# Kernel tuning notes

Measured on AMD Instinct MI355X. Metric: run time of the kernel, lower is better.

## Reference

```python
import jax, jax.numpy as jnp
import numpy as np

NUM_LATENTS = 1
NUM_EMBEDDINGS = 2048
EMBEDDING_DIM = 64
DECAY = 0.99
EPS = 1e-5


def setup_inputs() -> dict:
    key = jax.random.key(0)
    k1, k2 = jax.random.split(key)
    x = jax.random.normal(k1, (65536, NUM_LATENTS * EMBEDDING_DIM), dtype=jnp.float32)
    embedding = jax.random.normal(k2, (NUM_LATENTS, NUM_EMBEDDINGS, EMBEDDING_DIM), dtype=jnp.float32)
    cluster_size = jnp.ones((NUM_LATENTS, NUM_EMBEDDINGS), dtype=jnp.float32)
    return {"input": x, "embedding": embedding, "cluster_size": cluster_size}


def reference(input, embedding, cluster_size):
    L, K, D = embedding.shape
    flat = input.reshape(-1, L, D)  # (N, L, D)
    # Squared euclidean distances (N, L, K), expanded form of (x - e)^2 sum over D
    x_sq = jnp.sum(flat * flat, axis=-1, keepdims=True)           # (N, L, 1)
    e_sq = jnp.sum(embedding * embedding, axis=-1)[None]          # (1, L, K)
    cross = jnp.einsum('nld,lkd->nlk', flat, embedding)           # (N, L, K)
    distances = x_sq - 2.0 * cross + e_sq
    encoding_indices = jnp.argmin(distances, axis=-1)             # (N, L)
    # decode: gather codebook vectors
    quantized = embedding[jnp.arange(L)[None, :], encoding_indices]  # (N, L, D)
    encodings = jax.nn.one_hot(encoding_indices, K, dtype=input.dtype)  # (N, L, K)
    # --- EMA update (training branch, non-simple, laplace smoothing) ---
    onehot_sum = jnp.sum(encodings, axis=0)                       # (L, K)
    dw = jnp.einsum('nlk,nld->lkd', encodings, flat)              # (L, K, D)
    new_cluster_size = DECAY * cluster_size + (1.0 - DECAY) * onehot_sum
    n = jnp.sum(new_cluster_size, axis=-1, keepdims=True)
    cs = (new_cluster_size + EPS) / (n + K * EPS) * n
    new_embedding = DECAY * embedding + (1.0 - DECAY) * (dw / cs[..., None])
    # --- losses / outputs ---
    q = quantized.reshape(input.shape)
    commitment_loss = jnp.mean((q - input) ** 2)
    quantized_st = input + jax.lax.stop_gradient(q - input)
    avg_probs = jnp.mean(encodings, axis=0)                       # (L, K)
    perplexity = jnp.exp(-jnp.sum(avg_probs * jnp.log(avg_probs + 1e-10) / L))
    return (quantized_st, encodings, commitment_loss, perplexity, new_embedding, new_cluster_size)
```

## Files before the change

kernel.cpp:

```cpp
#include <hip/hip_runtime.h>
#include <math.h>

#define NROWS 65536
#define KEMB  2048
#define DIM   64
#define DECAYF 0.99f
#define OMDF   0.01f
#define EPSF   1e-5f

#define WS_DW    0
#define WS_CNT   131072
#define WS_LOSS  133120
#define WS_ESQ   133632
#define WS_IDX   137728
#define WS_SORT  203264
#define WS_START 268800
#define WS_CUR   270852

#define OUT_Q    0
#define OUT_ENC  4194304
#define OUT_LOSS 138412032
#define OUT_PERP 138412033
#define OUT_NE   138412034
#define OUT_NCS  138543106

typedef float f32x4 __attribute__((ext_vector_type(4)));

__global__ __launch_bounds__(256) void k0_prep(const float* __restrict__ E,
                                               float* __restrict__ ws) {
    int g = blockIdx.x * 256 + threadIdx.x;
    if (g == 0) ws[WS_LOSS] = 0.f;
    ((float4*)(ws + WS_DW))[g] = make_float4(0.f, 0.f, 0.f, 0.f);
    if (g < KEMB) {
        ((unsigned int*)ws)[WS_CNT + g] = 0u;
        const float4* e4 = (const float4*)(E + (size_t)g * DIM);
        float s0 = 0.f, s1 = 0.f, s2 = 0.f, s3 = 0.f;
#pragma unroll
        for (int j = 0; j < 16; j++) {
            float4 v = e4[j];
            s0 = fmaf(v.x, v.x, s0); s1 = fmaf(v.y, v.y, s1);
            s2 = fmaf(v.z, v.z, s2); s3 = fmaf(v.w, v.w, s3);
        }
        ws[WS_ESQ + g] = (s0 + s1) + (s2 + s3);
    }
}

__global__ __launch_bounds__(256, 3) void k1_main(const float* __restrict__ x,
                                                  const float* __restrict__ E,
                                                  float* __restrict__ ws,
                                                  float* __restrict__ out) {
    __shared__ float sxT[64 * 128];
    __shared__ float seT[16 * 256];
    __shared__ float sxq[256];

    const int t = threadIdx.x;
    const int b = blockIdx.x;
    const int tx = t & 15;
    const int ty = t >> 4;

    {
        const int rl = t & 127;
        const int dhi2 = t >> 7;
        const float4* x4 = (const float4*)x;
        float s0 = 0.f, s1 = 0.f, s2 = 0.f, s3 = 0.f;
#pragma unroll
        for (int i = 0; i < 8; i++) {
            int dc = dhi2 + 2 * i;
            float4 v = x4[((size_t)b * 128 + rl) * 16 + dc];
            sxT[(4 * dc + 0) * 128 + rl] = v.x;
            sxT[(4 * dc + 1) * 128 + rl] = v.y;
            sxT[(4 * dc + 2) * 128 + rl] = v.z;
            sxT[(4 * dc + 3) * 128 + rl] = v.w;
            s0 = fmaf(v.x, v.x, s0); s1 = fmaf(v.y, v.y, s1);
            s2 = fmaf(v.z, v.z, s2); s3 = fmaf(v.w, v.w, s3);
        }
        sxq[dhi2 * 128 + rl] = (s0 + s1) + (s2 + s3);
    }

    const int sbase = (((t >> 2) & 3) << 6) + ((t >> 4) << 2) + (t & 3);
    const float4* e4 = (const float4*)E;

    float4 pv[4];
#pragma unroll
    for (int j = 0; j < 4; j++)
        pv[j] = e4[(size_t)t * 16 + j];

    __syncthreads();

    float xsq[8];
#pragma unroll
    for (int rr = 0; rr < 8; rr++)
        xsq[rr] = sxq[ty * 8 + rr] + sxq[128 + ty * 8 + rr];

    float best[8];
    int bidx[8];
#pragma unroll
    for (int rr = 0; rr < 8; rr++) { best[rr] = 3.4e38f; bidx[rr] = 0; }

    f32x4* __restrict__ encz = (f32x4*)(out + OUT_ENC);

    for (int pass = 0; pass < 8; pass++) {
        float acc[8][16];
#pragma unroll
        for (int rr = 0; rr < 8; rr++)
#pragma unroll
            for (int m = 0; m < 16; m++) acc[rr][m] = 0.f;

        for (int q = 0; q < 4; q++) {
            if (pass + q) __syncthreads();
#pragma unroll
            for (int j = 0; j < 4; j++) {
                seT[(4 * j + 0) * 256 + sbase] = pv[j].x;
                seT[(4 * j + 1) * 256 + sbase] = pv[j].y;
                seT[(4 * j + 2) * 256 + sbase] = pv[j].z;
                seT[(4 * j + 3) * 256 + sbase] = pv[j].w;
            }
            __syncthreads();

            {
                int h = pass * 4 + q + 1;
                if (h < 32) {
#pragma unroll
                    for (int j = 0; j < 4; j++)
                        pv[j] = e4[((size_t)((h >> 2) * 256 + t)) * 16 + (h & 3) * 4 + j];
                }
            }

            {
                f32x4 z = (f32x4)(0.f);
#pragma unroll
                for (int j = 0; j < 8; j++)
                    __builtin_nontemporal_store(z,
                        encz + (size_t)b * 65536 + pass * 8192 + (q * 8 + j) * 256 + t);
            }

            const float* xbase = sxT + q * 16 * 128 + ty * 8;
            for (int dd = 0; dd < 16; dd++) {
                const float* sb = seT + dd * 256;
                f32x4 a0 = *(const f32x4*)(xbase + dd * 128);
                f32x4 a1 = *(const f32x4*)(xbase + dd * 128 + 4);
                f32x4 b0 = *(const f32x4*)(sb + tx * 4);
                f32x4 b1 = *(const f32x4*)(sb + 64 + tx * 4);
                f32x4 b2 = *(const f32x4*)(sb + 128 + tx * 4);
                f32x4 b3 = *(const f32x4*)(sb + 192 + tx * 4);
#pragma unroll
                for (int rr = 0; rr < 4; rr++) {
#pragma unroll
                    for (int cc = 0; cc < 4; cc++) {
                        acc[rr][cc]          = fmaf(a0[rr], b0[cc], acc[rr][cc]);
                        acc[rr][4 + cc]      = fmaf(a0[rr], b1[cc], acc[rr][4 + cc]);
                        acc[rr][8 + cc]      = fmaf(a0[rr], b2[cc], acc[rr][8 + cc]);
                        acc[rr][12 + cc]     = fmaf(a0[rr], b3[cc], acc[rr][12 + cc]);
                        acc[4 + rr][cc]      = fmaf(a1[rr], b0[cc], acc[4 + rr][cc]);
                        acc[4 + rr][4 + cc]  = fmaf(a1[rr], b1[cc], acc[4 + rr][4 + cc]);
                        acc[4 + rr][8 + cc]  = fmaf(a1[rr], b2[cc], acc[4 + rr][8 + cc]);
                        acc[4 + rr][12 + cc] = fmaf(a1[rr], b3[cc], acc[4 + rr][12 + cc]);
                    }
                }
            }
        }

        const float4* esq4 = (const float4*)(ws + WS_ESQ + pass * 256 + tx * 16);
        float4 eqv0 = esq4[0], eqv1 = esq4[1], eqv2 = esq4[2], eqv3 = esq4[3];
        float eq[16] = {eqv0.x, eqv0.y, eqv0.z, eqv0.w, eqv1.x, eqv1.y, eqv1.z, eqv1.w,
                        eqv2.x, eqv2.y, eqv2.z, eqv2.w, eqv3.x, eqv3.y, eqv3.z, eqv3.w};
        const int kb = pass * 256 + tx * 16;
#pragma unroll
        for (int rr = 0; rr < 8; rr++)
#pragma unroll
            for (int m = 0; m < 16; m++) {
                float dist = fmaf(-2.f, acc[rr][m], xsq[rr]) + eq[m];
                if (dist < best[rr]) { best[rr] = dist; bidx[rr] = kb + m; }
            }
    }

    int* sIdx = (int*)sxq;
#pragma unroll
    for (int rr = 0; rr < 8; rr++) {
        float bd = best[rr]; int bi = bidx[rr];
#pragma unroll
        for (int m = 1; m < 16; m <<= 1) {
            float od = __shfl_xor(bd, m, 64);
            int   oi = __shfl_xor(bi, m, 64);
            if (od < bd || (od == bd && oi < bi)) { bd = od; bi = oi; }
        }
        if (tx == 0) sIdx[ty * 8 + rr] = bi;
    }
    __syncthreads();

    if (t < 128) {
        const int row = b * 128 + t;
        const int bi = sIdx[t];
        ((int*)ws)[WS_IDX + row] = bi;
        atomicAdd(((unsigned int*)ws) + WS_CNT + bi, 1u);
        out[OUT_ENC + (size_t)row * KEMB + bi] = 1.0f;
        const float4* ebb = (const float4*)(E + (size_t)bi * DIM);
        const float4* xr4 = (const float4*)(x + (size_t)row * DIM);
        float4* qo = (float4*)(out + OUT_Q + (size_t)row * DIM);
        float l0 = 0.f, l1 = 0.f, l2 = 0.f, l3 = 0.f;
#pragma unroll
        for (int j = 0; j < 16; j++) {
            float4 ev = ebb[j];
            float4 xv = xr4[j];
            qo[j] = ev;
            float d0 = ev.x - xv.x, d1 = ev.y - xv.y;
            float d2 = ev.z - xv.z, d3 = ev.w - xv.w;
            l0 = fmaf(d0, d0, l0); l1 = fmaf(d1, d1, l1);
            l2 = fmaf(d2, d2, l2); l3 = fmaf(d3, d3, l3);
        }
        float lsum = (l0 + l1) + (l2 + l3);
#pragma unroll
        for (int o = 32; o; o >>= 1) lsum += __shfl_down(lsum, o, 64);
        if ((t & 63) == 0) unsafeAtomicAdd(ws + WS_LOSS, lsum);
    }
}

__global__ __launch_bounds__(256) void k2scan(float* __restrict__ ws) {
    __shared__ unsigned int sscan[256];
    const int t = threadIdx.x;
    const unsigned int* cnt = ((const unsigned int*)ws) + WS_CNT;
    unsigned int c[8];
    unsigned int tot = 0;
#pragma unroll
    for (int j = 0; j < 8; j++) { c[j] = cnt[t * 8 + j]; tot += c[j]; }
    sscan[t] = tot;
    __syncthreads();
    for (int off = 1; off < 256; off <<= 1) {
        unsigned int v = (t >= off) ? sscan[t - off] : 0u;
        __syncthreads();
        sscan[t] += v;
        __syncthreads();
    }
    unsigned int run = sscan[t] - tot;
    unsigned int* starts = ((unsigned int*)ws) + WS_START;
    unsigned int* cur = ((unsigned int*)ws) + WS_CUR;
#pragma unroll
    for (int j = 0; j < 8; j++) {
        starts[t * 8 + j] = run;
        cur[t * 8 + j] = run;
        run += c[j];
    }
    if (t == 255) starts[KEMB] = run;
}

__global__ __launch_bounds__(256) void k2c_scatter(const int* __restrict__ idxp,
                                                   float* __restrict__ ws) {
    const int g = blockIdx.x * 256 + threadIdx.x;
    const int code = idxp[g];
    unsigned int p = atomicAdd(((unsigned int*)ws) + WS_CUR + code, 1u);
    ((int*)ws)[WS_SORT + p] = g;
}

__global__ __launch_bounds__(256) void k2d_dw(const float* __restrict__ x,
                                              const int* __restrict__ idxp,
                                              float* __restrict__ ws) {
    const int t = threadIdx.x;
    const int lane = t & 63;
    const int w = blockIdx.x * 4 + (t >> 6);
    const int base = w * 32;
    const int* sorted = ((const int*)ws) + WS_SORT;

    int rid = (lane < 32) ? sorted[base + lane] : 0;
    int code_l = (lane < 32) ? idxp[rid] : 0;

    float acc = 0.f;
    int cur = __shfl(code_l, 0, 64);
#pragma unroll 8
    for (int i = 0; i < 32; i++) {
        int row = __shfl(rid, i, 64);
        int code = __shfl(code_l, i, 64);
        if (code != cur) {
            unsafeAtomicAdd(ws + WS_DW + (size_t)cur * DIM + lane, acc);
            acc = 0.f;
            cur = code;
        }
        acc += x[(size_t)row * DIM + lane];
    }
    unsafeAtomicAdd(ws + WS_DW + (size_t)cur * DIM + lane, acc);
}

__global__ __launch_bounds__(256) void k3_se(const float* __restrict__ cs_in,
                                             const float* __restrict__ E,
                                             const float* __restrict__ ws,
                                             float* __restrict__ out) {
    __shared__ float sred[8];
    __shared__ float sscale[16];
    __shared__ float s_n;
    const int t = threadIdx.x;
    const int b = blockIdx.x;
    const unsigned int* cnt = ((const unsigned int*)ws) + WS_CNT;

    float ln = 0.f, lent = 0.f;
#pragma unroll
    for (int j = 0; j < 8; j++) {
        int k = t * 8 + j;
        float c = (float)cnt[k];
        float ncs = DECAYF * cs_in[k] + OMDF * c;
        ln += ncs;
        float p = c * (1.0f / 65536.0f);
        lent = fmaf(p, logf(p + 1e-10f), lent);
    }
#pragma unroll
    for (int o = 32; o; o >>= 1) {
        ln += __shfl_down(ln, o, 64);
        lent += __shfl_down(lent, o, 64);
    }
    if ((t & 63) == 0) { sred[t >> 6] = ln; sred[4 + (t >> 6)] = lent; }
    __syncthreads();
    if (t == 0) {
        float n = (sred[0] + sred[1]) + (sred[2] + sred[3]);
        float ent = (sred[4] + sred[5]) + (sred[6] + sred[7]);
        s_n = n;
        if (b == 0) {
            out[OUT_LOSS] = ws[WS_LOSS] * (1.0f / 4194304.0f);
            out[OUT_PERP] = expf(-ent);
        }
    }
    __syncthreads();
    const float n = s_n;

    if (t < 16) {
        int k = b * 16 + t;
        float c = (float)cnt[k];
        float ncs = DECAYF * cs_in[k] + OMDF * c;
        out[OUT_NCS + k] = ncs;
        float cs = (ncs + EPSF) / (n + (float)KEMB * EPSF) * n;
        sscale[t] = OMDF / cs;
    }
    __syncthreads();

    const int k16 = t >> 4;
    const int d = (t & 15) * 4;
    const int k = b * 16 + k16;
    const float sc = sscale[k16];
    float4 e = ((const float4*)E)[k * 16 + (t & 15)];
    float4 dv = ((const float4*)(ws + WS_DW))[k * 16 + (t & 15)];
    float2 r0, r1;
    r0.x = fmaf(dv.x, sc, DECAYF * e.x);
    r0.y = fmaf(dv.y, sc, DECAYF * e.y);
    r1.x = fmaf(dv.z, sc, DECAYF * e.z);
    r1.y = fmaf(dv.w, sc, DECAYF * e.w);
    float2* o2 = (float2*)(out + OUT_NE);
    o2[(k * 64 + d) / 2 + 0] = r0;
    o2[(k * 64 + d) / 2 + 1] = r1;
}

extern "C" void kernel_launch(void* const* d_in, const int* in_sizes, int n_in,
                              void* d_out, int out_size, void* d_ws, size_t ws_size,
                              hipStream_t stream) {
    const float* x = (const float*)d_in[0];
    const float* E = (const float*)d_in[1];
    const float* cs = (const float*)d_in[2];
    float* out = (float*)d_out;
    float* ws = (float*)d_ws;
    const int* idxp = ((const int*)ws) + WS_IDX;

    hipLaunchKernelGGL(k0_prep, dim3(128), dim3(256), 0, stream, E, ws);
    hipLaunchKernelGGL(k1_main, dim3(512), dim3(256), 0, stream, x, E, ws, out);
    hipLaunchKernelGGL(k2scan, dim3(1), dim3(256), 0, stream, ws);
    hipLaunchKernelGGL(k2c_scatter, dim3(256), dim3(256), 0, stream, idxp, ws);
    hipLaunchKernelGGL(k2d_dw, dim3(512), dim3(256), 0, stream, x, idxp, ws);
    hipLaunchKernelGGL(k3_se, dim3(128), dim3(256), 0, stream, cs, E, ws, out);
}
```

Measured before the change: 340.3 us.

## Split codebook search across two blocks per row tile and merge in new kernel

The main distance kernel now launches twice as many blocks, and each block searches half of the codebook for its 128 rows. Each half writes its local best distance and index to scratch space (reusing the sort workspace and the new-embedding output region). A new finalize kernel picks the better half, then does the count atomics, one-hot write, quantized output and loss. The shared-memory codebook tile is also padded to 288 floats per row to reduce bank conflicts. This trades extra x loads, an extra launch and an extra scratch round-trip for more parallelism across the GPU's CUs.

New measurement: 355.1 us. +4.3%, slower.

```diff
diff --git a/kernel.cpp b/kernel.cpp
--- a/kernel.cpp
+++ b/kernel.cpp
@@ -50,11 +50,12 @@
                                                   float* __restrict__ ws,
                                                   float* __restrict__ out) {
     __shared__ float sxT[64 * 128];
-    __shared__ float seT[16 * 256];
+    __shared__ float seT[16 * 288];
     __shared__ float sxq[256];
 
     const int t = threadIdx.x;
-    const int b = blockIdx.x;
+    const int rb = blockIdx.x >> 1;
+    const int cb = blockIdx.x & 1;
     const int tx = t & 15;
     const int ty = t >> 4;
 
@@ -66,7 +67,7 @@
 #pragma unroll
         for (int i = 0; i < 8; i++) {
             int dc = dhi2 + 2 * i;
-            float4 v = x4[((size_t)b * 128 + rl) * 16 + dc];
+            float4 v = x4[((size_t)rb * 128 + rl) * 16 + dc];
             sxT[(4 * dc + 0) * 128 + rl] = v.x;
             sxT[(4 * dc + 1) * 128 + rl] = v.y;
             sxT[(4 * dc + 2) * 128 + rl] = v.z;
@@ -77,13 +78,13 @@
         sxq[dhi2 * 128 + rl] = (s0 + s1) + (s2 + s3);
     }
 
-    const int sbase = (((t >> 2) & 3) << 6) + ((t >> 4) << 2) + (t & 3);
+    const int sbase = ((t >> 2) & 3) * 72 + ((t >> 4) << 2) + (t & 3);
     const float4* e4 = (const float4*)E;
 
     float4 pv[4];
 #pragma unroll
     for (int j = 0; j < 4; j++)
-        pv[j] = e4[(size_t)t * 16 + j];
+        pv[j] = e4[(size_t)(cb * 1024 + t) * 16 + j];
 
     __syncthreads();
 
@@ -99,7 +100,7 @@
 
     f32x4* __restrict__ encz = (f32x4*)(out + OUT_ENC);
 
-    for (int pass = 0; pass < 8; pass++) {
+    for (int pass = 0; pass < 4; pass++) {
         float acc[8][16];
 #pragma unroll
         for (int rr = 0; rr < 8; rr++)
@@ -107,22 +108,23 @@
             for (int m = 0; m < 16; m++) acc[rr][m] = 0.f;
 
         for (int q = 0; q < 4; q++) {
-            if (pass + q) __syncthreads();
+            const int st = pass * 4 + q;
+            if (st) __syncthreads();
 #pragma unroll
             for (int j = 0; j < 4; j++) {
-                seT[(4 * j + 0) * 256 + sbase] = pv[j].x;
-                seT[(4 * j + 1) * 256 + sbase] = pv[j].y;
-                seT[(4 * j + 2) * 256 + sbase] = pv[j].z;
-                seT[(4 * j + 3) * 256 + sbase] = pv[j].w;
+                seT[(4 * j + 0) * 288 + sbase] = pv[j].x;
+                seT[(4 * j + 1) * 288 + sbase] = pv[j].y;
+                seT[(4 * j + 2) * 288 + sbase] = pv[j].z;
+                seT[(4 * j + 3) * 288 + sbase] = pv[j].w;
             }
             __syncthreads();
 
             {
-                int h = pass * 4 + q + 1;
-                if (h < 32) {
+                int h = st + 1;
+                if (h < 16) {
 #pragma unroll
                     for (int j = 0; j < 4; j++)
-                        pv[j] = e4[((size_t)((h >> 2) * 256 + t)) * 16 + (h & 3) * 4 + j];
+                        pv[j] = e4[(size_t)(cb * 1024 + (h >> 2) * 256 + t) * 16 + (h & 3) * 4 + j];
                 }
             }
 
@@ -131,18 +133,18 @@
 #pragma unroll
                 for (int j = 0; j < 8; j++)
                     __builtin_nontemporal_store(z,
-                        encz + (size_t)b * 65536 + pass * 8192 + (q * 8 + j) * 256 + t);
+                        encz + (size_t)(rb * 128 + st * 8 + j) * 512 + cb * 256 + t);
             }
 
             const float* xbase = sxT + q * 16 * 128 + ty * 8;
             for (int dd = 0; dd < 16; dd++) {
-                const float* sb = seT + dd * 256;
+                const float* sb = seT + dd * 288;
                 f32x4 a0 = *(const f32x4*)(xbase + dd * 128);
                 f32x4 a1 = *(const f32x4*)(xbase + dd * 128 + 4);
                 f32x4 b0 = *(const f32x4*)(sb + tx * 4);
-                f32x4 b1 = *(const f32x4*)(sb + 64 + tx * 4);
-                f32x4 b2 = *(const f32x4*)(sb + 128 + tx * 4);
-                f32x4 b3 = *(const f32x4*)(sb + 192 + tx * 4);
+                f32x4 b1 = *(const f32x4*)(sb + 72 + tx * 4);
+                f32x4 b2 = *(const f32x4*)(sb + 144 + tx * 4);
+                f32x4 b3 = *(const f32x4*)(sb + 216 + tx * 4);
 #pragma unroll
                 for (int rr = 0; rr < 4; rr++) {
 #pragma unroll
@@ -160,11 +162,11 @@
             }
         }
 
-        const float4* esq4 = (const float4*)(ws + WS_ESQ + pass * 256 + tx * 16);
+        const float4* esq4 = (const float4*)(ws + WS_ESQ + cb * 1024 + pass * 256 + tx * 16);
         float4 eqv0 = esq4[0], eqv1 = esq4[1], eqv2 = esq4[2], eqv3 = esq4[3];
         float eq[16] = {eqv0.x, eqv0.y, eqv0.z, eqv0.w, eqv1.x, eqv1.y, eqv1.z, eqv1.w,
                         eqv2.x, eqv2.y, eqv2.z, eqv2.w, eqv3.x, eqv3.y, eqv3.z, eqv3.w};
-        const int kb = pass * 256 + tx * 16;
+        const int kb = cb * 1024 + pass * 256 + tx * 16;
 #pragma unroll
         for (int rr = 0; rr < 8; rr++)
 #pragma unroll
@@ -175,6 +177,7 @@
     }
 
     int* sIdx = (int*)sxq;
+    float* sBest = sxq + 128;
 #pragma unroll
     for (int rr = 0; rr < 8; rr++) {
         float bd = best[rr]; int bi = bidx[rr];
@@ -184,35 +187,49 @@
             int   oi = __shfl_xor(bi, m, 64);
             if (od < bd || (od == bd && oi < bi)) { bd = od; bi = oi; }
         }
-        if (tx == 0) sIdx[ty * 8 + rr] = bi;
+        if (tx == 0) { sIdx[ty * 8 + rr] = bi; sBest[ty * 8 + rr] = bd; }
     }
     __syncthreads();
 
     if (t < 128) {
-        const int row = b * 128 + t;
-        const int bi = sIdx[t];
-        ((int*)ws)[WS_IDX + row] = bi;
-        atomicAdd(((unsigned int*)ws) + WS_CNT + bi, 1u);
-        out[OUT_ENC + (size_t)row * KEMB + bi] = 1.0f;
-        const float4* ebb = (const float4*)(E + (size_t)bi * DIM);
-        const float4* xr4 = (const float4*)(x + (size_t)row * DIM);
-        float4* qo = (float4*)(out + OUT_Q + (size_t)row * DIM);
-        float l0 = 0.f, l1 = 0.f, l2 = 0.f, l3 = 0.f;
-#pragma unroll
-        for (int j = 0; j < 16; j++) {
-            float4 ev = ebb[j];
-            float4 xv = xr4[j];
-            qo[j] = ev;
-            float d0 = ev.x - xv.x, d1 = ev.y - xv.y;
-            float d2 = ev.z - xv.z, d3 = ev.w - xv.w;
-            l0 = fmaf(d0, d0, l0); l1 = fmaf(d1, d1, l1);
-            l2 = fmaf(d2, d2, l2); l3 = fmaf(d3, d3, l3);
-        }
-        float lsum = (l0 + l1) + (l2 + l3);
-#pragma unroll
-        for (int o = 32; o; o >>= 1) lsum += __shfl_down(lsum, o, 64);
-        if ((t & 63) == 0) unsafeAtomicAdd(ws + WS_LOSS, lsum);
-    }
+        const int row = rb * 128 + t;
+        ((int*)ws)[(cb ? WS_SORT : WS_IDX) + row] = sIdx[t];
+        out[OUT_NE + cb * 65536 + row] = sBest[t];
+    }
+}
+
+__global__ __launch_bounds__(256) void k1b_fin(const float* __restrict__ x,
+                                               const float* __restrict__ E,
+                                               float* __restrict__ ws,
+                                               float* __restrict__ out) {
+    const int g = blockIdx.x * 256 + threadIdx.x;
+    float b0 = out[OUT_NE + g];
+    float b1 = out[OUT_NE + 65536 + g];
+    int i0 = ((int*)ws)[WS_IDX + g];
+    int i1 = ((int*)ws)[WS_SORT + g];
+    const int bi = (b1 < b0) ? i1 : i0;
+    ((int*)ws)[WS_IDX + g] = bi;
+    atomicAdd(((unsigned int*)ws) + WS_CNT + bi, 1u);
+    out[OUT_ENC + (size_t)g * KEMB + bi] = 1.0f;
+
+    const float4* ebb = (const float4*)(E + (size_t)bi * DIM);
+    const float4* xr4 = (const float4*)(x + (size_t)g * DIM);
+    float4* qo = (float4*)(out + OUT_Q + (size_t)g * DIM);
+    float l0 = 0.f, l1 = 0.f, l2 = 0.f, l3 = 0.f;
+#pragma unroll
+    for (int j = 0; j < 16; j++) {
+        float4 ev = ebb[j];
+        float4 xv = xr4[j];
+        qo[j] = ev;
+        float d0 = ev.x - xv.x, d1 = ev.y - xv.y;
+        float d2 = ev.z - xv.z, d3 = ev.w - xv.w;
+        l0 = fmaf(d0, d0, l0); l1 = fmaf(d1, d1, l1);
+        l2 = fmaf(d2, d2, l2); l3 = fmaf(d3, d3, l3);
+    }
+    float lsum = (l0 + l1) + (l2 + l3);
+#pragma unroll
+    for (int o = 32; o; o >>= 1) lsum += __shfl_down(lsum, o, 64);
+    if ((threadIdx.x & 63) == 0) unsafeAtomicAdd(ws + WS_LOSS, lsum);
 }
 
 __global__ __launch_bounds__(256) void k2scan(float* __restrict__ ws) {
@@ -356,7 +373,8 @@
     const int* idxp = ((const int*)ws) + WS_IDX;
 
     hipLaunchKernelGGL(k0_prep, dim3(128), dim3(256), 0, stream, E, ws);
-    hipLaunchKernelGGL(k1_main, dim3(512), dim3(256), 0, stream, x, E, ws, out);
+    hipLaunchKernelGGL(k1_main, dim3(1024), dim3(256), 0, stream, x, E, ws, out);
+    hipLaunchKernelGGL(k1b_fin, dim3(256), dim3(256), 0, stream, x, E, ws, out);
     hipLaunchKernelGGL(k2scan, dim3(1), dim3(256), 0, stream, ws);
     hipLaunchKernelGGL(k2c_scatter, dim3(256), dim3(256), 0, stream, idxp, ws);
     hipLaunchKernelGGL(k2d_dw, dim3(512), dim3(256), 0, stream, x, idxp, ws);
```
